# Optimization experiments

Hardware: AMD Instinct MI355X
Metric: run time of the kernel (lower is better)

Reference implementation:

```python
import jax, jax.numpy as jnp
import numpy as np

EPS = 1e-6
HQ, HKV, HD = 16, 4, 64   # num_q_heads, num_kv_heads, head_dim
TOPK = 2                  # num_exp_tokens
B, S, H, E, I = 2, 1024, 1024, 8, 2048


def _rms(x, w):
    return x * jax.lax.rsqrt(jnp.mean(x * x, -1, keepdims=True) + EPS) * w


def _rope(x, cos, sin):
    # x: [B,S,h,D]; cos/sin: [S,D/2]
    x1, x2 = jnp.split(x, 2, axis=-1)
    c = cos[None, :, None, :]
    s = sin[None, :, None, :]
    return jnp.concatenate([x1 * c - x2 * s, x1 * s + x2 * c], axis=-1)


def setup_inputs() -> dict:
    key = jax.random.key(0)
    ks = jax.random.split(key, 12)
    w = lambda k, sh: jax.random.normal(k, sh, jnp.float32) * 0.02
    return {
        "x": jax.random.normal(ks[0], (B, S, H), jnp.float32),
        "freq": jax.random.uniform(ks[1], (S, HD // 2), jnp.float32) * 6.28,
        "norm1_w": jnp.ones((H,), jnp.float32),
        "norm2_w": jnp.ones((H,), jnp.float32),
        "wq": w(ks[2], (H, HQ * HD)),
        "wk": w(ks[3], (H, HKV * HD)),
        "wv": w(ks[4], (H, HKV * HD)),
        "wo": w(ks[5], (HQ * HD, H)),
        "qn_w": jnp.ones((HD,), jnp.float32),
        "kn_w": jnp.ones((HD,), jnp.float32),
        "gate_w": w(ks[6], (H, E)),
        "w1": w(ks[7], (E, H, I)),
        "w2": w(ks[8], (E, I, H)),
        "w3": w(ks[9], (E, H, I)),
    }


def reference(x, freq, norm1_w, norm2_w, wq, wk, wv, wo, qn_w, kn_w,
              gate_w, w1, w2, w3):
    b, s, h = x.shape
    # ---- GQA attention with qk_norm + RoPE ----
    hn = _rms(x, norm1_w)
    q = (hn @ wq).reshape(b, s, HQ, HD)
    k = (hn @ wk).reshape(b, s, HKV, HD)
    v = (hn @ wv).reshape(b, s, HKV, HD)
    q = _rms(q, qn_w)
    k = _rms(k, kn_w)
    cos, sin = jnp.cos(freq), jnp.sin(freq)
    q = _rope(q, cos, sin)
    k = _rope(k, cos, sin)
    rep = HQ // HKV
    kr = jnp.repeat(k, rep, axis=2)  # [b,s,HQ,HD]
    vr = jnp.repeat(v, rep, axis=2)
    scores = jnp.einsum('bqhd,bkhd->bhqk', q, kr) * (HD ** -0.5)
    mask = jnp.tril(jnp.ones((s, s), bool))
    scores = jnp.where(mask, scores, jnp.finfo(scores.dtype).min)
    att = jax.nn.softmax(scores, axis=-1)
    y = jnp.einsum('bhqk,bkhd->bqhd', att, vr).reshape(b, s, HQ * HD) @ wo
    x = x + y

    # ---- Sparse MoE FFN (top-k softmax gate, SwiGLU experts) ----
    t = _rms(x, norm2_w).reshape(b * s, h)
    probs = jax.nn.softmax(t @ gate_w, axis=-1)          # [T,E]
    vals, idx = jax.lax.top_k(probs, TOPK)               # [T,k]
    vals = vals / jnp.sum(vals, -1, keepdims=True)       # renormalize top-k
    T = b * s
    combine = jnp.zeros((T, E), t.dtype).at[
        jnp.arange(T)[:, None], idx].add(vals)           # [T,E]
    u = jnp.einsum('th,ehi->eti', t, w1)
    g = jax.nn.silu(u) * jnp.einsum('th,ehi->eti', t, w3)
    ye = jnp.einsum('eti,eih->eth', g, w2)               # [E,T,H]
    moe = jnp.einsum('eth,te->th', ye, combine).reshape(b, s, h)
    return (x + moe, k, v)
```

## Files before the change

### kernel.cpp

```cpp
#include <hip/hip_runtime.h>
#include <hip/hip_bf16.h>

#define HQn 16
#define HKVn 4
#define HDn 64
#define Bn 2
#define Sn 1024
#define Hn 1024
#define En 8
#define In 2048
#define Tn 2048
#define EPSf 1e-6f

typedef __attribute__((ext_vector_type(8))) short bf16x8;
typedef __attribute__((ext_vector_type(4))) float f32x4;

__device__ __forceinline__ unsigned short f2bf(float f) {
  unsigned u = __float_as_uint(f);
  u += 0x7fffu + ((u >> 16) & 1u);
  return (unsigned short)(u >> 16);
}
__device__ __forceinline__ float bf2f(unsigned short u) {
  return __uint_as_float(((unsigned)u) << 16);
}
__device__ __forceinline__ void gll16(const void* g, void* l) {
  __builtin_amdgcn_global_load_lds(
      (const __attribute__((address_space(1))) void*)g,
      (__attribute__((address_space(3))) void*)l, 16, 0, 0);
}

__global__ __launch_bounds__(256) void k_tcvt(
    const float* __restrict__ src, unsigned short* __restrict__ dst,
    int R, int C, size_t sZ, size_t dZ) {
  src += (size_t)blockIdx.z * sZ;
  dst += (size_t)blockIdx.z * dZ;
  int c0 = blockIdx.x * 64, r0 = blockIdx.y * 64;
  __shared__ float t[64][65];
  int tid = threadIdx.x;
  int lr = tid >> 4, lc = (tid & 15) * 4;
#pragma unroll
  for (int p = 0; p < 4; p++) {
    float4 v = *(const float4*)(src + (size_t)(r0 + lr + p * 16) * C + c0 + lc);
    t[lr + p * 16][lc + 0] = v.x; t[lr + p * 16][lc + 1] = v.y;
    t[lr + p * 16][lc + 2] = v.z; t[lr + p * 16][lc + 3] = v.w;
  }
  __syncthreads();
  int oc = tid >> 2;
  int seg = (tid & 3) * 16;
  unsigned pk[8];
#pragma unroll
  for (int j = 0; j < 8; j++) {
    unsigned short lo = f2bf(t[seg + 2 * j][oc]);
    unsigned short hi = f2bf(t[seg + 2 * j + 1][oc]);
    pk[j] = (unsigned)lo | ((unsigned)hi << 16);
  }
  uint4* dp = (uint4*)(dst + (size_t)(c0 + oc) * R + r0 + seg);
  dp[0] = make_uint4(pk[0], pk[1], pk[2], pk[3]);
  dp[1] = make_uint4(pk[4], pk[5], pk[6], pk[7]);
}

__global__ __launch_bounds__(256) void k_tcvt2(
    const float* __restrict__ src, unsigned short* __restrict__ dsth,
    unsigned short* __restrict__ dstl, int R, int C) {
  int c0 = blockIdx.x * 64, r0 = blockIdx.y * 64;
  __shared__ float t[64][65];
  int tid = threadIdx.x;
  int lr = tid >> 4, lc = (tid & 15) * 4;
#pragma unroll
  for (int p = 0; p < 4; p++) {
    float4 v = *(const float4*)(src + (size_t)(r0 + lr + p * 16) * C + c0 + lc);
    t[lr + p * 16][lc + 0] = v.x; t[lr + p * 16][lc + 1] = v.y;
    t[lr + p * 16][lc + 2] = v.z; t[lr + p * 16][lc + 3] = v.w;
  }
  __syncthreads();
  int oc = tid >> 2;
  int seg = (tid & 3) * 16;
  unsigned pkh[8], pkl[8];
#pragma unroll
  for (int j = 0; j < 8; j++) {
    float a = t[seg + 2 * j][oc], b = t[seg + 2 * j + 1][oc];
    unsigned short ahh = f2bf(a), bhh = f2bf(b);
    unsigned short alo = f2bf(a - bf2f(ahh)), blo = f2bf(b - bf2f(bhh));
    pkh[j] = (unsigned)ahh | ((unsigned)bhh << 16);
    pkl[j] = (unsigned)alo | ((unsigned)blo << 16);
  }
  size_t db = (size_t)(c0 + oc) * R + r0 + seg;
  uint4* dph = (uint4*)(dsth + db);
  dph[0] = make_uint4(pkh[0], pkh[1], pkh[2], pkh[3]);
  dph[1] = make_uint4(pkh[4], pkh[5], pkh[6], pkh[7]);
  uint4* dpl = (uint4*)(dstl + db);
  dpl[0] = make_uint4(pkl[0], pkl[1], pkl[2], pkl[3]);
  dpl[1] = make_uint4(pkl[4], pkl[5], pkl[6], pkl[7]);
}

__global__ __launch_bounds__(256) void k_rmsnorm(
    const float* __restrict__ x, const float* __restrict__ w,
    unsigned short* __restrict__ outh, unsigned short* __restrict__ outl) {
  int row = blockIdx.x, tid = threadIdx.x;
  size_t off = (size_t)row * Hn + tid * 4;
  float4 v = *(const float4*)(x + off);
  float ss = v.x * v.x + v.y * v.y + v.z * v.z + v.w * v.w;
#pragma unroll
  for (int o = 32; o > 0; o >>= 1) ss += __shfl_xor(ss, o);
  __shared__ float ls[4];
  if ((tid & 63) == 0) ls[tid >> 6] = ss;
  __syncthreads();
  float tot = ls[0] + ls[1] + ls[2] + ls[3];
  float sc = rsqrtf(tot * (1.0f / Hn) + EPSf);
  float4 wv = *(const float4*)(w + tid * 4);
  float o0 = v.x * sc * wv.x, o1 = v.y * sc * wv.y;
  float o2 = v.z * sc * wv.z, o3 = v.w * sc * wv.w;
  ushort4 h4, l4;
  h4.x = f2bf(o0); l4.x = f2bf(o0 - bf2f(h4.x));
  h4.y = f2bf(o1); l4.y = f2bf(o1 - bf2f(h4.y));
  h4.z = f2bf(o2); l4.z = f2bf(o2 - bf2f(h4.z));
  h4.w = f2bf(o3); l4.w = f2bf(o3 - bf2f(h4.w));
  *(ushort4*)(outh + off) = h4;
  *(ushort4*)(outl + off) = l4;
}

__global__ __launch_bounds__(256) void k_resid_norm(
    const float* __restrict__ x, const float* __restrict__ y,
    const float* __restrict__ w, float* __restrict__ x2out,
    float* __restrict__ tout, unsigned short* __restrict__ tbf) {
  int row = blockIdx.x, tid = threadIdx.x;
  size_t off = (size_t)row * Hn + tid * 4;
  float4 xv = *(const float4*)(x + off);
  float4 yv = *(const float4*)(y + off);
  float4 s;
  s.x = xv.x + yv.x; s.y = xv.y + yv.y; s.z = xv.z + yv.z; s.w = xv.w + yv.w;
  *(float4*)(x2out + off) = s;
  float ss = s.x * s.x + s.y * s.y + s.z * s.z + s.w * s.w;
#pragma unroll
  for (int o = 32; o > 0; o >>= 1) ss += __shfl_xor(ss, o);
  __shared__ float ls[4];
  if ((tid & 63) == 0) ls[tid >> 6] = ss;
  __syncthreads();
  float tot = ls[0] + ls[1] + ls[2] + ls[3];
  float sc = rsqrtf(tot * (1.0f / Hn) + EPSf);
  float4 wv4 = *(const float4*)(w + tid * 4);
  float4 t4;
  t4.x = s.x * sc * wv4.x; t4.y = s.y * sc * wv4.y;
  t4.z = s.z * sc * wv4.z; t4.w = s.w * sc * wv4.w;
  *(float4*)(tout + off) = t4;
  ushort4 b4;
  b4.x = f2bf(t4.x); b4.y = f2bf(t4.y); b4.z = f2bf(t4.z); b4.w = f2bf(t4.w);
  *(ushort4*)(tbf + off) = b4;
}

template<int MT>
__global__ __launch_bounds__(256) void k_pgemm(
    const unsigned short* __restrict__ Ah, const unsigned short* __restrict__ Al,
    const unsigned short* __restrict__ Bth, const unsigned short* __restrict__ Btl,
    float* __restrict__ C, int N, int K) {
  constexpr int BM = MT * 32;
  constexpr int ASL = BM * 32;
  __shared__ __align__(16) short smAh[2][ASL], smAl[2][ASL];
  __shared__ __align__(16) short smBh[2][4096], smBl[2][4096];
  int tid = threadIdx.x, wave = tid >> 6, lane = tid & 63;
  int n0 = blockIdx.x * 128, m0 = blockIdx.y * BM;
  int wm = wave >> 1, wn = wave & 1;
  int r0 = ((tid >> 6) << 4) | (tid & 15);
  int k0 = ((tid >> 4) & 3) * 8;
  int r1 = r0 + 64;
  const unsigned short* pAh0 = Ah + (size_t)(m0 + r0) * K + k0;
  const unsigned short* pAl0 = Al + (size_t)(m0 + r0) * K + k0;
  const unsigned short* pBh0 = Bth + (size_t)(n0 + r0) * K + k0;
  const unsigned short* pBl0 = Btl + (size_t)(n0 + r0) * K + k0;
  const unsigned short* pBh1 = Bth + (size_t)(n0 + r1) * K + k0;
  const unsigned short* pBl1 = Btl + (size_t)(n0 + r1) * K + k0;
  const unsigned short* pAh1 = pAh0;
  const unsigned short* pAl1 = pAl0;
  if constexpr (MT == 4) {
    pAh1 = Ah + (size_t)(m0 + r1) * K + k0;
    pAl1 = Al + (size_t)(m0 + r1) * K + k0;
  }
  int d0 = tid * 8, d1 = (256 + tid) * 8;
  auto STAGE = [&](int b, int kb) {
    gll16(pAh0 + kb, &smAh[b][d0]);
    gll16(pAl0 + kb, &smAl[b][d0]);
    if constexpr (MT == 4) {
      gll16(pAh1 + kb, &smAh[b][d1]);
      gll16(pAl1 + kb, &smAl[b][d1]);
    }
    gll16(pBh0 + kb, &smBh[b][d0]);
    gll16(pBl0 + kb, &smBl[b][d0]);
    gll16(pBh1 + kb, &smBh[b][d1]);
    gll16(pBl1 + kb, &smBl[b][d1]);
  };
  f32x4 zf = {0.f, 0.f, 0.f, 0.f};
  f32x4 acc[MT][4];
#pragma unroll
  for (int i = 0; i < MT; i++)
#pragma unroll
    for (int j = 0; j < 4; j++) acc[i][j] = zf;
  STAGE(0, 0);
  __syncthreads();
  for (int kb = 0; kb < K; kb += 32) {
    int cur = (kb >> 5) & 1;
    if (kb + 32 < K) STAGE(cur ^ 1, kb + 32);
    bf16x8 ah[MT], al[MT], bh[4], bl[4];
#pragma unroll
    for (int i = 0; i < MT; i++) {
      ah[i] = *(const bf16x8*)&smAh[cur][((wm * MT + i) * 64 + lane) * 8];
      al[i] = *(const bf16x8*)&smAl[cur][((wm * MT + i) * 64 + lane) * 8];
    }
#pragma unroll
    for (int j = 0; j < 4; j++) {
      bh[j] = *(const bf16x8*)&smBh[cur][((wn * 4 + j) * 64 + lane) * 8];
      bl[j] = *(const bf16x8*)&smBl[cur][((wn * 4 + j) * 64 + lane) * 8];
    }
#pragma unroll
    for (int i = 0; i < MT; i++)
#pragma unroll
      for (int j = 0; j < 4; j++) {
        acc[i][j] = __builtin_amdgcn_mfma_f32_16x16x32_bf16(ah[i], bh[j], acc[i][j], 0, 0, 0);
        acc[i][j] = __builtin_amdgcn_mfma_f32_16x16x32_bf16(ah[i], bl[j], acc[i][j], 0, 0, 0);
        acc[i][j] = __builtin_amdgcn_mfma_f32_16x16x32_bf16(al[i], bh[j], acc[i][j], 0, 0, 0);
      }
    __syncthreads();
  }
  int cr = (lane >> 4) * 4, cc = lane & 15;
#pragma unroll
  for (int i = 0; i < MT; i++) {
    int row0 = m0 + (wm * MT + i) * 16 + cr;
#pragma unroll
    for (int j = 0; j < 4; j++) {
      int col = n0 + (wn * 4 + j) * 16 + cc;
#pragma unroll
      for (int r = 0; r < 4; r++)
        C[(size_t)(row0 + r) * N + col] = acc[i][j][r];
    }
  }
}

__global__ __launch_bounds__(256) void k_qkv_post(
    const float* __restrict__ qkv, const float* __restrict__ qn_w,
    const float* __restrict__ kn_w, const float* __restrict__ freq,
    float* __restrict__ q_t,
    unsigned short* __restrict__ kT8h, unsigned short* __restrict__ kT8l,
    unsigned short* __restrict__ vT8h, unsigned short* __restrict__ vT8l,
    float* __restrict__ k_out, float* __restrict__ v_out) {
  int gw = blockIdx.x * 4 + (threadIdx.x >> 6);
  int lane = threadIdx.x & 63;
  int token = gw / 24;
  int hh = gw % 24;
  int b = token / Sn, s = token % Sn;
  if (hh >= 20) {
    int h = hh - 20;
    float v = qkv[(size_t)token * 1536 + 1280 + h * HDn + lane];
    unsigned short hi = f2bf(v);
    unsigned short lo = f2bf(v - bf2f(hi));
    size_t vb = (((size_t)(b * HKVn + h) * 128 + (s >> 3)) * 64 + lane) * 8 + (s & 7);
    vT8h[vb] = hi; vT8l[vb] = lo;
    v_out[(size_t)token * (HKVn * HDn) + h * HDn + lane] = v;
    return;
  }
  bool isq = hh < 16;
  int h = isq ? hh : hh - 16;
  float val = isq ? qkv[(size_t)token * 1536 + h * HDn + lane]
                  : qkv[(size_t)token * 1536 + 1024 + h * HDn + lane];
  float ss = val * val;
#pragma unroll
  for (int o = 32; o > 0; o >>= 1) ss += __shfl_xor(ss, o);
  float scn = rsqrtf(ss * (1.0f / HDn) + EPSf);
  float w = isq ? qn_w[lane] : kn_w[lane];
  float xn = val * scn * w;
  float f = freq[(size_t)s * (HDn / 2) + (lane & 31)];
  float c = cosf(f), sn = sinf(f);
  float partner = __shfl_xor(xn, 32);
  float out = (lane < 32) ? (xn * c - partner * sn) : (partner * sn + xn * c);
  if (isq) {
    q_t[(((size_t)(b * HQn + h)) * Sn + s) * HDn + lane] = out;
  } else {
    unsigned short hi = f2bf(out);
    unsigned short lo = f2bf(out - bf2f(hi));
    size_t kb = (((size_t)(b * HKVn + h) * 8 + (lane >> 3)) * Sn + s) * 8 + (lane & 7);
    kT8h[kb] = hi; kT8l[kb] = lo;
    k_out[(size_t)token * (HKVn * HDn) + h * HDn + lane] = out;
  }
}

__global__ __launch_bounds__(256) void k_attn_mfma(
    const float* __restrict__ q_t,
    const unsigned short* __restrict__ kT8h, const unsigned short* __restrict__ kT8l,
    const unsigned short* __restrict__ vT8h, const unsigned short* __restrict__ vT8l,
    unsigned short* __restrict__ yh, unsigned short* __restrict__ yl) {
  __shared__ __align__(16) unsigned short klh[4096], kll[4096];
  __shared__ __align__(16) unsigned short vth[4096], vtl[4096];
  __shared__ __align__(16) unsigned short Ph[4][1152], Pl[4][1152];
  int bid = blockIdx.x;
  int qt = 63 - (bid & 63);
  int kvh = (bid >> 6) & 3;
  int b = bid >> 8;
  int tid = threadIdx.x, w = tid >> 6, lane = tid & 63;
  int h = kvh * 4 + w;
  int g = lane >> 4, li = lane & 15;
  const float* qrow = q_t + (((size_t)(b * HQn + h) * Sn) + qt * 16 + li) * HDn + g * 8;
  bf16x8 qh[2], ql[2];
#pragma unroll
  for (int kc = 0; kc < 2; kc++) {
    float v[8];
    *(float4*)(v) = *(const float4*)(qrow + kc * 32);
    *(float4*)(v + 4) = *(const float4*)(qrow + kc * 32 + 4);
#pragma unroll
    for (int j = 0; j < 8; j++) {
      unsigned short hi = f2bf(v[j]);
      qh[kc][j] = (short)hi;
      ql[kc][j] = (short)f2bf(v[j] - bf2f(hi));
    }
  }
  size_t bh = (size_t)(b * HKVn + kvh) * 65536;
  f32x4 acc[4];
  f32x4 zf = {0.f, 0.f, 0.f, 0.f};
#pragma unroll
  for (int nt = 0; nt < 4; nt++) acc[nt] = zf;
  float m_[4] = {-1e30f, -1e30f, -1e30f, -1e30f};
  float l_[4] = {0.f, 0.f, 0.f, 0.f};
  int rowb = qt * 16 + g * 4;
  int kmax = qt * 16 + 15;
  for (int kk = 0; kk <= kmax; kk += 64) {
    __syncthreads();
#pragma unroll
    for (int i = 0; i < 2; i++) {
      int idx = w * 2 + i;
      gll16(kT8h + bh + (size_t)idx * 8192 + (size_t)kk * 8 + lane * 8, &klh[idx * 512]);
      gll16(kT8l + bh + (size_t)idx * 8192 + (size_t)kk * 8 + lane * 8, &kll[idx * 512]);
      gll16(vT8h + bh + (size_t)(kk / 8 + idx) * 512 + lane * 8, &vth[idx * 512]);
      gll16(vT8l + bh + (size_t)(kk / 8 + idx) * 512 + lane * 8, &vtl[idx * 512]);
    }
    __syncthreads();
    f32x4 st[4];
#pragma unroll
    for (int kt = 0; kt < 4; kt++) st[kt] = zf;
#pragma unroll
    for (int kt = 0; kt < 4; kt++)
#pragma unroll
      for (int kc = 0; kc < 2; kc++) {
        int ko = (kc * 4 + g) * 512 + (kt * 16 + li) * 8;
        bf16x8 kh = *(const bf16x8*)&klh[ko];
        bf16x8 klo = *(const bf16x8*)&kll[ko];
        st[kt] = __builtin_amdgcn_mfma_f32_16x16x32_bf16(qh[kc], kh, st[kt], 0, 0, 0);
        st[kt] = __builtin_amdgcn_mfma_f32_16x16x32_bf16(qh[kc], klo, st[kt], 0, 0, 0);
        st[kt] = __builtin_amdgcn_mfma_f32_16x16x32_bf16(ql[kc], kh, st[kt], 0, 0, 0);
      }
    float mx[4] = {-1e30f, -1e30f, -1e30f, -1e30f};
#pragma unroll
    for (int kt = 0; kt < 4; kt++) {
      int key = kk + kt * 16 + li;
#pragma unroll
      for (int r = 0; r < 4; r++) {
        float s = st[kt][r] * 0.125f;
        if (key > rowb + r) s = -1e30f;
        st[kt][r] = s;
        mx[r] = fmaxf(mx[r], s);
      }
    }
#pragma unroll
    for (int r = 0; r < 4; r++) {
#pragma unroll
      for (int o = 1; o < 16; o <<= 1) mx[r] = fmaxf(mx[r], __shfl_xor(mx[r], o));
      float mn = fmaxf(m_[r], mx[r]);
      mx[r] = __expf(m_[r] - mn);
      m_[r] = mn;
    }
    float rs[4] = {0.f, 0.f, 0.f, 0.f};
#pragma unroll
    for (int kt = 0; kt < 4; kt++)
#pragma unroll
      for (int r = 0; r < 4; r++) {
        float p = __expf(st[kt][r] - m_[r]);
        rs[r] += p;
        unsigned short phh = f2bf(p);
        Ph[w][(g * 4 + r) * 72 + kt * 16 + li] = phh;
        Pl[w][(g * 4 + r) * 72 + kt * 16 + li] = f2bf(p - bf2f(phh));
      }
#pragma unroll
    for (int r = 0; r < 4; r++) {
#pragma unroll
      for (int o = 1; o < 16; o <<= 1) rs[r] += __shfl_xor(rs[r], o);
      l_[r] = l_[r] * mx[r] + rs[r];
#pragma unroll
      for (int nt = 0; nt < 4; nt++) acc[nt][r] *= mx[r];
    }
    bf16x8 pfh[2], pfl[2];
#pragma unroll
    for (int kc = 0; kc < 2; kc++) {
      int po = li * 72 + kc * 32 + g * 8;
      pfh[kc] = *(const bf16x8*)&Ph[w][po];
      pfl[kc] = *(const bf16x8*)&Pl[w][po];
    }
#pragma unroll
    for (int nt = 0; nt < 4; nt++)
#pragma unroll
      for (int kc = 0; kc < 2; kc++) {
        int vo = (kc * 4 + g) * 512 + (nt * 16 + li) * 8;
        bf16x8 vh = *(const bf16x8*)&vth[vo];
        bf16x8 vl = *(const bf16x8*)&vtl[vo];
        acc[nt] = __builtin_amdgcn_mfma_f32_16x16x32_bf16(pfh[kc], vh, acc[nt], 0, 0, 0);
        acc[nt] = __builtin_amdgcn_mfma_f32_16x16x32_bf16(pfh[kc], vl, acc[nt], 0, 0, 0);
        acc[nt] = __builtin_amdgcn_mfma_f32_16x16x32_bf16(pfl[kc], vh, acc[nt], 0, 0, 0);
      }
  }
  size_t ybase = ((size_t)(b * Sn) + qt * 16) * (HQn * HDn) + h * HDn;
#pragma unroll
  for (int r = 0; r < 4; r++) {
    float inv = 1.f / l_[r];
#pragma unroll
    for (int nt = 0; nt < 4; nt++) {
      size_t idx = ybase + (size_t)(g * 4 + r) * (HQn * HDn) + nt * 16 + li;
      float v = acc[nt][r] * inv;
      unsigned short hi = f2bf(v);
      yh[idx] = hi;
      yl[idx] = f2bf(v - bf2f(hi));
    }
  }
}

__global__ __launch_bounds__(256) void k_router(
    const float* __restrict__ t, const float* __restrict__ gw_,
    int* __restrict__ idx, float* __restrict__ val, int* __restrict__ cnt) {
  int tok = blockIdx.x * 4 + (threadIdx.x >> 6);
  int lane = threadIdx.x & 63;
  const float* tr = t + (size_t)tok * Hn;
  float s[8] = {0, 0, 0, 0, 0, 0, 0, 0};
  for (int hh = lane; hh < Hn; hh += 64) {
    float tv = tr[hh];
    float4 g0 = *(const float4*)(gw_ + hh * 8);
    float4 g1 = *(const float4*)(gw_ + hh * 8 + 4);
    s[0] = fmaf(tv, g0.x, s[0]); s[1] = fmaf(tv, g0.y, s[1]);
    s[2] = fmaf(tv, g0.z, s[2]); s[3] = fmaf(tv, g0.w, s[3]);
    s[4] = fmaf(tv, g1.x, s[4]); s[5] = fmaf(tv, g1.y, s[5]);
    s[6] = fmaf(tv, g1.z, s[6]); s[7] = fmaf(tv, g1.w, s[7]);
  }
#pragma unroll
  for (int e = 0; e < 8; e++)
#pragma unroll
    for (int off = 32; off > 0; off >>= 1) s[e] += __shfl_xor(s[e], off);
  if (lane == 0) {
    float mx = s[0];
    for (int e = 1; e < 8; e++) mx = fmaxf(mx, s[e]);
    float p[8];
    for (int e = 0; e < 8; e++) p[e] = __expf(s[e] - mx);
    int e0 = 0;
    for (int e = 1; e < 8; e++) if (p[e] > p[e0]) e0 = e;
    int e1 = (e0 == 0) ? 1 : 0;
    for (int e = 0; e < 8; e++) if (e != e0 && p[e] > p[e1]) e1 = e;
    float v0 = p[e0], v1 = p[e1], inv = 1.f / (v0 + v1);
    idx[tok * 2] = e0; idx[tok * 2 + 1] = e1;
    val[tok * 2] = v0 * inv; val[tok * 2 + 1] = v1 * inv;
    atomicAdd(&cnt[e0], 1); atomicAdd(&cnt[e1], 1);
  }
}

__global__ void k_scan(const int* __restrict__ cnt, int* __restrict__ offs,
                       int* __restrict__ cursor) {
  if (threadIdx.x == 0) {
    int run = 0;
    for (int e = 0; e < En; e++) { offs[e] = run; cursor[e] = run; run += cnt[e]; }
  }
}

__global__ __launch_bounds__(256) void k_scatter(
    const int* __restrict__ idx, const float* __restrict__ val,
    int* __restrict__ cursor, int* __restrict__ tokl, float* __restrict__ wvl) {
  int t = blockIdx.x * 256 + threadIdx.x;
#pragma unroll
  for (int slot = 0; slot < 2; slot++) {
    int e = idx[t * 2 + slot];
    int pos = atomicAdd(&cursor[e], 1);
    tokl[pos] = t;
    wvl[pos] = val[t * 2 + slot];
  }
}

__global__ __launch_bounds__(256) void k_gather(
    const unsigned short* __restrict__ tb, const int* __restrict__ tokl,
    unsigned short* __restrict__ tg) {
  int r = blockIdx.x;
  int tk = tokl[r];
  const ushort4* s = (const ushort4*)(tb + (size_t)tk * Hn);
  ushort4* d = (ushort4*)(tg + (size_t)r * Hn);
  d[threadIdx.x] = s[threadIdx.x];
}

__global__ __launch_bounds__(512) void k_moe13(
    const unsigned short* __restrict__ tg, const unsigned short* __restrict__ w13t,
    unsigned short* __restrict__ ug, const int* __restrict__ cnt,
    const int* __restrict__ offs) {
  int e = blockIdx.z;
  int n_e = cnt[e];
  int mt = blockIdx.y;
  if (mt * 256 >= n_e) return;
  int base = offs[e];
  int n0 = blockIdx.x * 256;
  const unsigned short* A = tg + (size_t)(base + mt * 256) * Hn;
  const unsigned short* Bt = w13t + (size_t)e * (2 * In) * Hn + (size_t)n0 * Hn;
  __shared__ __align__(16) short sA0[16384], sA1[16384];
  __shared__ __align__(16) short sB0[16384], sB1[16384];
  int tid = threadIdx.x;
  int wave = tid >> 6, lane = tid & 63;
  int wm = wave >> 2, wn = wave & 3;
  int rowLo = ((tid >> 6) << 4) | (tid & 15);
  int kLo = ((tid >> 4) & 3) * 8;
  const unsigned short* a0 = A + (size_t)rowLo * Hn + kLo;
  const unsigned short* a1 = A + (size_t)(rowLo + 128) * Hn + kLo;
  const unsigned short* b0 = Bt + (size_t)rowLo * Hn + kLo;
  const unsigned short* b1 = Bt + (size_t)(rowLo + 128) * Hn + kLo;
  size_t d0 = (size_t)tid * 8;
#define M13_STAGE(S, kb) do { \
    gll16(a0 + (kb), sA##S + d0); \
    gll16(a1 + (kb), sA##S + 4096 + d0); \
    gll16(a0 + (kb) + 32, sA##S + 8192 + d0); \
    gll16(a1 + (kb) + 32, sA##S + 12288 + d0); \
    gll16(b0 + (kb), sB##S + d0); \
    gll16(b1 + (kb), sB##S + 4096 + d0); \
    gll16(b0 + (kb) + 32, sB##S + 8192 + d0); \
    gll16(b1 + (kb) + 32, sB##S + 12288 + d0); \
  } while (0)
#define M13_COMP(S) do { \
    _Pragma("unroll") \
    for (int kk = 0; kk < 2; kk++) { \
      bf16x8 af[8], bfr[4]; \
      _Pragma("unroll") \
      for (int i = 0; i < 8; i++) \
        af[i] = *(const bf16x8*)(sA##S + kk * 8192 + ((wm * 8 + i) * 64 + lane) * 8); \
      _Pragma("unroll") \
      for (int j = 0; j < 4; j++) \
        bfr[j] = *(const bf16x8*)(sB##S + kk * 8192 + ((wn * 4 + j) * 64 + lane) * 8); \
      _Pragma("unroll") \
      for (int i = 0; i < 8; i++) \
        _Pragma("unroll") \
        for (int j = 0; j < 4; j++) \
          acc[i][j] = __builtin_amdgcn_mfma_f32_16x16x32_bf16(af[i], bfr[j], acc[i][j], 0, 0, 0); \
    } \
  } while (0)
  f32x4 zf = {0.f, 0.f, 0.f, 0.f};
  f32x4 acc[8][4];
#pragma unroll
  for (int i = 0; i < 8; i++)
#pragma unroll
    for (int j = 0; j < 4; j++) acc[i][j] = zf;
  M13_STAGE(0, 0);
  __syncthreads();
  for (int kb = 0; kb < Hn; kb += 128) {
    M13_STAGE(1, kb + 64);
    M13_COMP(0);
    __syncthreads();
    if (kb + 128 < Hn) M13_STAGE(0, kb + 128);
    M13_COMP(1);
    __syncthreads();
  }
#undef M13_STAGE
#undef M13_COMP
  int cr = (lane >> 4) * 4, cc = lane & 15;
#pragma unroll
  for (int i = 0; i < 8; i++) {
    int lrow0 = wm * 128 + i * 16 + cr;
#pragma unroll
    for (int j = 0; j < 4; j++) {
      int ncol = n0 + wn * 64 + j * 16 + cc;
#pragma unroll
      for (int r = 0; r < 4; r++) {
        int rr = mt * 256 + lrow0 + r;
        if (rr < n_e)
          ug[(size_t)(base + rr) * (2 * In) + ncol] = f2bf(acc[i][j][r]);
      }
    }
  }
}

__global__ __launch_bounds__(256) void k_act(
    const unsigned short* __restrict__ ug, unsigned short* __restrict__ act) {
  size_t p = ((size_t)blockIdx.x * 256 + threadIdx.x) * 8;
  size_t r = p >> 11;
  int c = (int)(p & 2047);
  const ushort4* up = (const ushort4*)(ug + r * 4096 + c);
  const ushort4* gp = (const ushort4*)(ug + r * 4096 + 2048 + c);
  ushort4* ap = (ushort4*)(act + r * 2048 + c);
#pragma unroll
  for (int h = 0; h < 2; h++) {
    ushort4 uu = up[h], gg = gp[h];
    ushort4 oo;
    float u0 = bf2f(uu.x), u1 = bf2f(uu.y), u2 = bf2f(uu.z), u3 = bf2f(uu.w);
    oo.x = f2bf(u0 / (1.f + __expf(-u0)) * bf2f(gg.x));
    oo.y = f2bf(u1 / (1.f + __expf(-u1)) * bf2f(gg.y));
    oo.z = f2bf(u2 / (1.f + __expf(-u2)) * bf2f(gg.z));
    oo.w = f2bf(u3 / (1.f + __expf(-u3)) * bf2f(gg.w));
    ap[h] = oo;
  }
}

__global__ __launch_bounds__(512) void k_moe2(
    const unsigned short* __restrict__ act, const unsigned short* __restrict__ w2t,
    const int* __restrict__ cnt, const int* __restrict__ offs,
    const int* __restrict__ tokl, const float* __restrict__ wvl,
    float* __restrict__ out0) {
  int e = blockIdx.z;
  int n_e = cnt[e];
  int mt = blockIdx.y;
  if (mt * 128 >= n_e) return;
  int base = offs[e];
  __shared__ int ltok[128];
  __shared__ float lwv[128];
  int tid = threadIdx.x;
  if (tid < 128) {
    int rr = mt * 128 + tid;
    bool v = rr < n_e;
    ltok[tid] = v ? tokl[base + rr] : -1;
    lwv[tid] = v ? wvl[base + rr] : 0.f;
  }
  const unsigned short* A = act + (size_t)(base + mt * 128) * In;
  const unsigned short* Bt = w2t + (size_t)e * Hn * In;
  __shared__ __align__(16) short smA[2][4096];
  __shared__ __align__(16) short smB[2][4096];
  int wave = tid >> 6, lane = tid & 63;
  int n0 = blockIdx.x * 128;
  int wm = wave >> 1, wn = wave & 1;
  int r0s = ((tid >> 6) << 4) | (tid & 15);
  int k0s = ((tid >> 4) & 3) * 8;
  const unsigned short* ApA = A + (size_t)r0s * In + k0s;
  const unsigned short* BpB = Bt + (size_t)(n0 + r0s) * In + k0s;
  auto STAGE = [&](int b, int kb) {
    gll16(ApA + kb, &smA[b][tid * 8]);
    gll16(BpB + kb, &smB[b][tid * 8]);
  };
  f32x4 zf = {0.f, 0.f, 0.f, 0.f};
  f32x4 acc[2][4];
#pragma unroll
  for (int i = 0; i < 2; i++)
#pragma unroll
    for (int j = 0; j < 4; j++) acc[i][j] = zf;
  STAGE(0, 0);
  __syncthreads();
  for (int kb = 0; kb < In; kb += 32) {
    int cur = (kb >> 5) & 1;
    if (kb + 32 < In) STAGE(cur ^ 1, kb + 32);
    bf16x8 af[2], bfr[4];
#pragma unroll
    for (int i = 0; i < 2; i++)
      af[i] = *(const bf16x8*)&smA[cur][((wm * 2 + i) * 64 + lane) * 8];
#pragma unroll
    for (int j = 0; j < 4; j++)
      bfr[j] = *(const bf16x8*)&smB[cur][((wn * 4 + j) * 64 + lane) * 8];
#pragma unroll
    for (int i = 0; i < 2; i++)
#pragma unroll
      for (int j = 0; j < 4; j++)
        acc[i][j] = __builtin_amdgcn_mfma_f32_16x16x32_bf16(af[i], bfr[j], acc[i][j], 0, 0, 0);
    __syncthreads();
  }
  int cr = (lane >> 4) * 4, cc = lane & 15;
#pragma unroll
  for (int i = 0; i < 2; i++) {
    int lrow0 = wm * 32 + i * 16 + cr;
#pragma unroll
    for (int j = 0; j < 4; j++) {
      int ncol = n0 + wn * 64 + j * 16 + cc;
#pragma unroll
      for (int r = 0; r < 4; r++) {
        int lrow = lrow0 + r;
        int tk = ltok[lrow];
        if (tk >= 0)
          atomicAdd(out0 + (size_t)tk * Hn + ncol, lwv[lrow] * acc[i][j][r]);
      }
    }
  }
}

extern "C" void kernel_launch(void* const* d_in, const int* in_sizes, int n_in,
                              void* d_out, int out_size, void* d_ws, size_t ws_size,
                              hipStream_t stream) {
  (void)in_sizes; (void)n_in; (void)out_size; (void)ws_size;
  const float* x      = (const float*)d_in[0];
  const float* freq   = (const float*)d_in[1];
  const float* n1w    = (const float*)d_in[2];
  const float* n2w    = (const float*)d_in[3];
  const float* wq     = (const float*)d_in[4];
  const float* wk     = (const float*)d_in[5];
  const float* wvp    = (const float*)d_in[6];
  const float* wo     = (const float*)d_in[7];
  const float* qn_w   = (const float*)d_in[8];
  const float* kn_w   = (const float*)d_in[9];
  const float* gate_w = (const float*)d_in[10];
  const float* w1     = (const float*)d_in[11];
  const float* w2     = (const float*)d_in[12];
  const float* w3     = (const float*)d_in[13];

  float* out0  = (float*)d_out;
  float* k_out = out0 + (size_t)Tn * Hn;
  float* v_out = k_out + (size_t)Tn * HKVn * HDn;

  char* wsb = (char*)d_ws;
  unsigned short* w13t = (unsigned short*)(wsb + 0);
  unsigned short* w2t  = (unsigned short*)(wsb + 67108864);
  unsigned short* tbf  = (unsigned short*)(wsb + 100663296);
  unsigned short* tg   = (unsigned short*)(wsb + 104857600);
  unsigned short* wqkvt_h = (unsigned short*)(wsb + 113246208);
  unsigned short* wqkvt_l = (unsigned short*)(wsb + 116391936);
  unsigned short* wot_h   = (unsigned short*)(wsb + 119537664);
  unsigned short* wot_l   = (unsigned short*)(wsb + 121634816);
  unsigned short* act  = (unsigned short*)(wsb + 113246208);
  unsigned short* hnh  = (unsigned short*)(wsb + 130023424);
  unsigned short* hnl  = (unsigned short*)(wsb + 134217728);
  float* qkv_raw = (float*)(wsb + 138412032);
  float* q_t   = (float*)(wsb + 150994944);
  unsigned short* kT8h = (unsigned short*)(wsb + 159383552);
  unsigned short* kT8l = (unsigned short*)(wsb + 160432128);
  unsigned short* vT8h = (unsigned short*)(wsb + 161480704);
  unsigned short* vT8l = (unsigned short*)(wsb + 162529280);
  unsigned short* ug = (unsigned short*)(wsb + 130023424);
  unsigned short* yh = (unsigned short*)(wsb + 163577856);
  unsigned short* yl = (unsigned short*)(wsb + 167772160);
  float* y2    = (float*)(wsb + 171966464);
  float* t_norm = (float*)(wsb + 150994944);
  char*  rtr   = wsb + 180355072;
  int*   idxb   = (int*)(rtr);
  float* valb   = (float*)(rtr + 16384);
  int*   cnt    = (int*)(rtr + 32768);
  int*   offs   = (int*)(rtr + 32768 + 128);
  int*   cursor = (int*)(rtr + 32768 + 256);
  int*   tokl   = (int*)(rtr + 32768 + 384);
  float* wvl    = (float*)(rtr + 32768 + 384 + 16384);

  k_tcvt<<<dim3(32, 16, 8), 256, 0, stream>>>(w1, w13t, 1024, 2048,
                                              (size_t)1024 * 2048, (size_t)4096 * 1024);
  k_tcvt<<<dim3(32, 16, 8), 256, 0, stream>>>(w3, w13t + (size_t)2048 * 1024, 1024, 2048,
                                              (size_t)1024 * 2048, (size_t)4096 * 1024);
  k_tcvt<<<dim3(16, 32, 8), 256, 0, stream>>>(w2, w2t, 2048, 1024,
                                              (size_t)2048 * 1024, (size_t)1024 * 2048);
  k_tcvt2<<<dim3(16, 16), 256, 0, stream>>>(wq, wqkvt_h, wqkvt_l, 1024, 1024);
  k_tcvt2<<<dim3(4, 16), 256, 0, stream>>>(wk, wqkvt_h + (size_t)1024 * 1024,
                                           wqkvt_l + (size_t)1024 * 1024, 1024, 256);
  k_tcvt2<<<dim3(4, 16), 256, 0, stream>>>(wvp, wqkvt_h + (size_t)1280 * 1024,
                                           wqkvt_l + (size_t)1280 * 1024, 1024, 256);
  k_tcvt2<<<dim3(16, 16), 256, 0, stream>>>(wo, wot_h, wot_l, 1024, 1024);

  hipMemsetAsync(cnt, 0, 8 * sizeof(int), stream);

  k_rmsnorm<<<Tn, 256, 0, stream>>>(x, n1w, hnh, hnl);
  k_pgemm<4><<<dim3(12, 16), 256, 0, stream>>>(hnh, hnl, wqkvt_h, wqkvt_l,
                                               qkv_raw, 1536, 1024);
  k_qkv_post<<<(Tn * 24) / 4, 256, 0, stream>>>(qkv_raw, qn_w, kn_w,
                                                freq, q_t, kT8h, kT8l, vT8h, vT8l,
                                                k_out, v_out);
  k_attn_mfma<<<Bn * HKVn * 64, 256, 0, stream>>>(q_t, kT8h, kT8l, vT8h, vT8l, yh, yl);
  k_pgemm<2><<<dim3(8, 32), 256, 0, stream>>>(yh, yl, wot_h, wot_l, y2, 1024, 1024);
  k_resid_norm<<<Tn, 256, 0, stream>>>(x, y2, n2w, out0, t_norm, tbf);
  k_router<<<Tn / 4, 256, 0, stream>>>(t_norm, gate_w, idxb, valb, cnt);
  k_scan<<<1, 64, 0, stream>>>(cnt, offs, cursor);
  k_scatter<<<Tn / 256, 256, 0, stream>>>(idxb, valb, cursor, tokl, wvl);
  k_gather<<<2 * Tn, 256, 0, stream>>>(tbf, tokl, tg);
  k_moe13<<<dim3(16, 8, 8), 512, 0, stream>>>(tg, w13t, ug, cnt, offs);
  k_act<<<4096, 256, 0, stream>>>(ug, act);
  k_moe2<<<dim3(8, 16, 8), 512, 0, stream>>>(act, w2t, cnt, offs, tokl, wvl, out0);
}
```

Baseline: 679.5 us.

## Deepen GEMM prefetch with vmcnt-based waits and raw barriers across three kernels

Rewrites the main loops of the split-precision projection GEMM, the MoE up-projection and the MoE down-projection so that two LDS stages are in flight. Each kernel now waits on a partial s_waitcnt vmcnt count and a bare s_barrier instead of __syncthreads, which lets the next tile's global-to-LDS loads overlap the current compute. The down-projection also doubles its K step to 64 per stage. The goal is to hide global load latency and cut barrier stalls. In exchange the code relies on hand-tuned wait counts and uses more LDS, which may lower occupancy and risks races if a count is wrong.

```diff
diff --git a/kernel.cpp b/kernel.cpp
--- a/kernel.cpp
+++ b/kernel.cpp
@@ -28,6 +28,13 @@
       (const __attribute__((address_space(1))) void*)g,
       (__attribute__((address_space(3))) void*)l, 16, 0, 0);
 }
+template<int N> __device__ __forceinline__ void vmw() {
+  if constexpr (N == 0) asm volatile("s_waitcnt vmcnt(0)" ::: "memory");
+  else if constexpr (N == 4) asm volatile("s_waitcnt vmcnt(4)" ::: "memory");
+  else if constexpr (N == 6) asm volatile("s_waitcnt vmcnt(6)" ::: "memory");
+  else if constexpr (N == 8) asm volatile("s_waitcnt vmcnt(8)" ::: "memory");
+}
+#define BARRIER() __builtin_amdgcn_s_barrier()
 
 __global__ __launch_bounds__(256) void k_tcvt(
     const float* __restrict__ src, unsigned short* __restrict__ dst,
@@ -153,73 +160,84 @@
     const unsigned short* __restrict__ Ah, const unsigned short* __restrict__ Al,
     const unsigned short* __restrict__ Bth, const unsigned short* __restrict__ Btl,
     float* __restrict__ C, int N, int K) {
-  constexpr int BM = MT * 32;
-  constexpr int ASL = BM * 32;
-  __shared__ __align__(16) short smAh[2][ASL], smAl[2][ASL];
-  __shared__ __align__(16) short smBh[2][4096], smBl[2][4096];
+  constexpr int ASL = MT * 1024;
+  constexpr int NLD = (MT == 4) ? 8 : 6;
+  __shared__ __align__(16) short sAh0[ASL], sAh1[ASL], sAl0[ASL], sAl1[ASL];
+  __shared__ __align__(16) short sBh0[4096], sBh1[4096], sBl0[4096], sBl1[4096];
   int tid = threadIdx.x, wave = tid >> 6, lane = tid & 63;
-  int n0 = blockIdx.x * 128, m0 = blockIdx.y * BM;
+  int n0 = blockIdx.x * 128, m0 = blockIdx.y * MT * 32;
   int wm = wave >> 1, wn = wave & 1;
   int r0 = ((tid >> 6) << 4) | (tid & 15);
   int k0 = ((tid >> 4) & 3) * 8;
   int r1 = r0 + 64;
-  const unsigned short* pAh0 = Ah + (size_t)(m0 + r0) * K + k0;
-  const unsigned short* pAl0 = Al + (size_t)(m0 + r0) * K + k0;
+  const unsigned short* pAh = Ah + (size_t)(m0 + r0) * K + k0;
+  const unsigned short* pAl = Al + (size_t)(m0 + r0) * K + k0;
   const unsigned short* pBh0 = Bth + (size_t)(n0 + r0) * K + k0;
   const unsigned short* pBl0 = Btl + (size_t)(n0 + r0) * K + k0;
   const unsigned short* pBh1 = Bth + (size_t)(n0 + r1) * K + k0;
   const unsigned short* pBl1 = Btl + (size_t)(n0 + r1) * K + k0;
-  const unsigned short* pAh1 = pAh0;
-  const unsigned short* pAl1 = pAl0;
+  const unsigned short* pAh1 = pAh;
+  const unsigned short* pAl1 = pAl;
   if constexpr (MT == 4) {
     pAh1 = Ah + (size_t)(m0 + r1) * K + k0;
     pAl1 = Al + (size_t)(m0 + r1) * K + k0;
   }
-  int d0 = tid * 8, d1 = (256 + tid) * 8;
-  auto STAGE = [&](int b, int kb) {
-    gll16(pAh0 + kb, &smAh[b][d0]);
-    gll16(pAl0 + kb, &smAl[b][d0]);
-    if constexpr (MT == 4) {
-      gll16(pAh1 + kb, &smAh[b][d1]);
-      gll16(pAl1 + kb, &smAl[b][d1]);
-    }
-    gll16(pBh0 + kb, &smBh[b][d0]);
-    gll16(pBl0 + kb, &smBl[b][d0]);
-    gll16(pBh1 + kb, &smBh[b][d1]);
-    gll16(pBl1 + kb, &smBl[b][d1]);
-  };
+  size_t d0 = (size_t)tid * 8, d1 = (size_t)(256 + tid) * 8;
+#define PG_STAGE(S, kb) do { \
+    gll16(pAh + (kb), sAh##S + d0); \
+    gll16(pAl + (kb), sAl##S + d0); \
+    if constexpr (MT == 4) { \
+      gll16(pAh1 + (kb), sAh##S + d1); \
+      gll16(pAl1 + (kb), sAl##S + d1); \
+    } \
+    gll16(pBh0 + (kb), sBh##S + d0); \
+    gll16(pBl0 + (kb), sBl##S + d0); \
+    gll16(pBh1 + (kb), sBh##S + d1); \
+    gll16(pBl1 + (kb), sBl##S + d1); \
+  } while (0)
+#define PG_COMP(S) do { \
+    bf16x8 ah[MT], al[MT], bh[4], bl[4]; \
+    _Pragma("unroll") \
+    for (int i = 0; i < MT; i++) { \
+      ah[i] = *(const bf16x8*)(sAh##S + ((wm * MT + i) * 64 + lane) * 8); \
+      al[i] = *(const bf16x8*)(sAl##S + ((wm * MT + i) * 64 + lane) * 8); \
+    } \
+    _Pragma("unroll") \
+    for (int j = 0; j < 4; j++) { \
+      bh[j] = *(const bf16x8*)(sBh##S + ((wn * 4 + j) * 64 + lane) * 8); \
+      bl[j] = *(const bf16x8*)(sBl##S + ((wn * 4 + j) * 64 + lane) * 8); \
+    } \
+    _Pragma("unroll") \
+    for (int i = 0; i < MT; i++) \
+      _Pragma("unroll") \
+      for (int j = 0; j < 4; j++) { \
+        acc[i][j] = __builtin_amdgcn_mfma_f32_16x16x32_bf16(ah[i], bh[j], acc[i][j], 0, 0, 0); \
+        acc[i][j] = __builtin_amdgcn_mfma_f32_16x16x32_bf16(ah[i], bl[j], acc[i][j], 0, 0, 0); \
+        acc[i][j] = __builtin_amdgcn_mfma_f32_16x16x32_bf16(al[i], bh[j], acc[i][j], 0, 0, 0); \
+      } \
+  } while (0)
   f32x4 zf = {0.f, 0.f, 0.f, 0.f};
   f32x4 acc[MT][4];
 #pragma unroll
   for (int i = 0; i < MT; i++)
 #pragma unroll
     for (int j = 0; j < 4; j++) acc[i][j] = zf;
-  STAGE(0, 0);
-  __syncthreads();
-  for (int kb = 0; kb < K; kb += 32) {
-    int cur = (kb >> 5) & 1;
-    if (kb + 32 < K) STAGE(cur ^ 1, kb + 32);
-    bf16x8 ah[MT], al[MT], bh[4], bl[4];
-#pragma unroll
-    for (int i = 0; i < MT; i++) {
-      ah[i] = *(const bf16x8*)&smAh[cur][((wm * MT + i) * 64 + lane) * 8];
-      al[i] = *(const bf16x8*)&smAl[cur][((wm * MT + i) * 64 + lane) * 8];
-    }
-#pragma unroll
-    for (int j = 0; j < 4; j++) {
-      bh[j] = *(const bf16x8*)&smBh[cur][((wn * 4 + j) * 64 + lane) * 8];
-      bl[j] = *(const bf16x8*)&smBl[cur][((wn * 4 + j) * 64 + lane) * 8];
-    }
-#pragma unroll
-    for (int i = 0; i < MT; i++)
-#pragma unroll
-      for (int j = 0; j < 4; j++) {
-        acc[i][j] = __builtin_amdgcn_mfma_f32_16x16x32_bf16(ah[i], bh[j], acc[i][j], 0, 0, 0);
-        acc[i][j] = __builtin_amdgcn_mfma_f32_16x16x32_bf16(ah[i], bl[j], acc[i][j], 0, 0, 0);
-        acc[i][j] = __builtin_amdgcn_mfma_f32_16x16x32_bf16(al[i], bh[j], acc[i][j], 0, 0, 0);
-      }
-    __syncthreads();
-  }
+  PG_STAGE(0, 0);
+  PG_STAGE(1, 32);
+  vmw<NLD>();
+  BARRIER();
+  for (int kb = 0; kb < K; kb += 64) {
+    PG_COMP(0);
+    BARRIER();
+    if (kb + 64 < K) { PG_STAGE(0, kb + 64); vmw<NLD>(); } else { vmw<0>(); }
+    BARRIER();
+    PG_COMP(1);
+    BARRIER();
+    if (kb + 96 < K) { PG_STAGE(1, kb + 96); vmw<NLD>(); } else { vmw<0>(); }
+    BARRIER();
+  }
+#undef PG_STAGE
+#undef PG_COMP
   int cr = (lane >> 4) * 4, cc = lane & 15;
 #pragma unroll
   for (int i = 0; i < MT; i++) {
@@ -542,14 +560,18 @@
 #pragma unroll
     for (int j = 0; j < 4; j++) acc[i][j] = zf;
   M13_STAGE(0, 0);
-  __syncthreads();
+  M13_STAGE(1, 64);
+  vmw<8>();
+  BARRIER();
   for (int kb = 0; kb < Hn; kb += 128) {
-    M13_STAGE(1, kb + 64);
     M13_COMP(0);
-    __syncthreads();
-    if (kb + 128 < Hn) M13_STAGE(0, kb + 128);
+    BARRIER();
+    if (kb + 128 < Hn) { M13_STAGE(0, kb + 128); vmw<8>(); } else { vmw<0>(); }
+    BARRIER();
     M13_COMP(1);
-    __syncthreads();
+    BARRIER();
+    if (kb + 192 < Hn) { M13_STAGE(1, kb + 192); vmw<8>(); } else { vmw<0>(); }
+    BARRIER();
   }
 #undef M13_STAGE
 #undef M13_COMP
@@ -610,46 +632,64 @@
     ltok[tid] = v ? tokl[base + rr] : -1;
     lwv[tid] = v ? wvl[base + rr] : 0.f;
   }
+  __syncthreads();
   const unsigned short* A = act + (size_t)(base + mt * 128) * In;
   const unsigned short* Bt = w2t + (size_t)e * Hn * In;
-  __shared__ __align__(16) short smA[2][4096];
-  __shared__ __align__(16) short smB[2][4096];
+  __shared__ __align__(16) short sA0[8192], sA1[8192];
+  __shared__ __align__(16) short sB0[8192], sB1[8192];
   int wave = tid >> 6, lane = tid & 63;
   int n0 = blockIdx.x * 128;
   int wm = wave >> 1, wn = wave & 1;
   int r0s = ((tid >> 6) << 4) | (tid & 15);
   int k0s = ((tid >> 4) & 3) * 8;
-  const unsigned short* ApA = A + (size_t)r0s * In + k0s;
-  const unsigned short* BpB = Bt + (size_t)(n0 + r0s) * In + k0s;
-  auto STAGE = [&](int b, int kb) {
-    gll16(ApA + kb, &smA[b][tid * 8]);
-    gll16(BpB + kb, &smB[b][tid * 8]);
-  };
+  const unsigned short* a0 = A + (size_t)r0s * In + k0s;
+  const unsigned short* b0 = Bt + (size_t)(n0 + r0s) * In + k0s;
+  size_t d0 = (size_t)tid * 8;
+#define M2_STAGE(S, kb) do { \
+    gll16(a0 + (kb), sA##S + d0); \
+    gll16(a0 + (kb) + 32, sA##S + 4096 + d0); \
+    gll16(b0 + (kb), sB##S + d0); \
+    gll16(b0 + (kb) + 32, sB##S + 4096 + d0); \
+  } while (0)
+#define M2_COMP(S) do { \
+    _Pragma("unroll") \
+    for (int kk = 0; kk < 2; kk++) { \
+      bf16x8 af[2], bfr[4]; \
+      _Pragma("unroll") \
+      for (int i = 0; i < 2; i++) \
+        af[i] = *(const bf16x8*)(sA##S + kk * 4096 + ((wm * 2 + i) * 64 + lane) * 8); \
+      _Pragma("unroll") \
+      for (int j = 0; j < 4; j++) \
+        bfr[j] = *(const bf16x8*)(sB##S + kk * 4096 + ((wn * 4 + j) * 64 + lane) * 8); \
+      _Pragma("unroll") \
+      for (int i = 0; i < 2; i++) \
+        _Pragma("unroll") \
+        for (int j = 0; j < 4; j++) \
+          acc[i][j] = __builtin_amdgcn_mfma_f32_16x16x32_bf16(af[i], bfr[j], acc[i][j], 0, 0, 0); \
+    } \
+  } while (0)
   f32x4 zf = {0.f, 0.f, 0.f, 0.f};
   f32x4 acc[2][4];
 #pragma unroll
   for (int i = 0; i < 2; i++)
 #pragma unroll
     for (int j = 0; j < 4; j++) acc[i][j] = zf;
-  STAGE(0, 0);
-  __syncthreads();
-  for (int kb = 0; kb < In; kb += 32) {
-    int cur = (kb >> 5) & 1;
-    if (kb + 32 < In) STAGE(cur ^ 1, kb + 32);
-    bf16x8 af[2], bfr[4];
-#pragma unroll
-    for (int i = 0; i < 2; i++)
-      af[i] = *(const bf16x8*)&smA[cur][((wm * 2 + i) * 64 + lane) * 8];
-#pragma unroll
-    for (int j = 0; j < 4; j++)
-      bfr[j] = *(const bf16x8*)&smB[cur][((wn * 4 + j) * 64 + lane) * 8];
-#pragma unroll
-    for (int i = 0; i < 2; i++)
-#pragma unroll
-      for (int j = 0; j < 4; j++)
-        acc[i][j] = __builtin_amdgcn_mfma_f32_16x16x32_bf16(af[i], bfr[j], acc[i][j], 0, 0, 0);
-    __syncthreads();
-  }
+  M2_STAGE(0, 0);
+  M2_STAGE(1, 64);
+  vmw<4>();
+  BARRIER();
+  for (int kb = 0; kb < In; kb += 128) {
+    M2_COMP(0);
+    BARRIER();
+    if (kb + 128 < In) { M2_STAGE(0, kb + 128); vmw<4>(); } else { vmw<0>(); }
+    BARRIER();
+    M2_COMP(1);
+    BARRIER();
+    if (kb + 192 < In) { M2_STAGE(1, kb + 192); vmw<4>(); } else { vmw<0>(); }
+    BARRIER();
+  }
+#undef M2_STAGE
+#undef M2_COMP
   int cr = (lane >> 4) * 4, cc = lane & 15;
 #pragma unroll
   for (int i = 0; i < 2; i++) {
```

Measured after the change: 669.1 us. About the same (-1.5%).
